# Optimization experiments

Hardware: AMD Instinct MI355X
Metric: run time of the kernel (lower is better)

Reference implementation:

```python
import jax, jax.numpy as jnp
import numpy as np

N = 50000
E = 625000
D = 128
L = 3
BN_EPS = 1e-5


def setup_inputs() -> dict:
    key = jax.random.key(0)
    ks = jax.random.split(key, 12)
    x = jax.random.normal(ks[0], (N, D), dtype=jnp.float32)
    edge_index = jax.random.randint(ks[1], (2, E), 0, N, dtype=jnp.int64)
    s = 1.0 / np.sqrt(D)
    W1 = jax.random.uniform(ks[2], (L, D, D), jnp.float32, -s, s)
    b1 = jax.random.uniform(ks[3], (L, D), jnp.float32, -s, s)
    W2 = jax.random.uniform(ks[4], (L, D, D), jnp.float32, -s, s)
    b2 = jax.random.uniform(ks[5], (L, D), jnp.float32, -s, s)
    eps = jnp.zeros((L,), jnp.float32)  # GINConv train_eps init 0
    gamma = jnp.ones((L, D), jnp.float32)
    beta = jnp.zeros((L, D), jnp.float32)
    Wl = jax.random.uniform(ks[6], (L, D, D), jnp.float32, -s, s)
    bl = jax.random.uniform(ks[7], (L, D), jnp.float32, -s, s)
    return {"x": x, "edge_index": edge_index, "W1": W1, "b1": b1, "W2": W2,
            "b2": b2, "eps": eps, "gamma": gamma, "beta": beta, "Wl": Wl, "bl": bl}


def reference(x, edge_index, W1, b1, W2, b2, eps, gamma, beta, Wl, bl):
    src, dst = edge_index[0], edge_index[1]
    xs = [x]
    h = x
    for i in range(L):
        # GIN aggregation: sum of neighbor (source) features at target nodes
        agg = jax.ops.segment_sum(h[src], dst, num_segments=N)  # [N, D]
        z = (1.0 + eps[i]) * h + agg
        # MLP: Linear -> ReLU -> Linear
        z = jax.nn.relu(z @ W1[i] + b1[i]) @ W2[i] + b2[i]
        # BatchNorm1d (training mode: batch stats, biased variance)
        mu = jnp.mean(z, axis=0)
        var = jnp.mean((z - mu) ** 2, axis=0)
        z = gamma[i] * (z - mu) * jax.lax.rsqrt(var + BN_EPS) + beta[i]
        if i != 0:
            z = z + xs[-1]
        h = jax.nn.relu(z)
        xs.append(h)
    outs = [xs[i + 1] @ Wl[i] + bl[i] for i in range(L)]
    return jnp.concatenate(outs, axis=-1)  # [N, L*D]
```

## Files before the change

kernel.cpp:

```cpp
#include <hip/hip_runtime.h>
#include <hip/hip_bf16.h>
#include <stdint.h>

#define NN 50000
#define NE 625000
#define DD 128
#define NL 3
#define GB 391

typedef __bf16 bf16x8 __attribute__((ext_vector_type(8)));
typedef float f32x4 __attribute__((ext_vector_type(4)));

__device__ __forceinline__ float bflo(uint32_t u) { return __uint_as_float(u << 16); }
__device__ __forceinline__ float bfhi(uint32_t u) { return __uint_as_float(u & 0xffff0000u); }
__device__ __forceinline__ uint16_t f2bf(float f) {
    __hip_bfloat16 h = __float2bfloat16(f);
    return __builtin_bit_cast(uint16_t, h);
}
__device__ __forceinline__ uint32_t pack2(float lo, float hi) {
    return (uint32_t)f2bf(lo) | ((uint32_t)f2bf(hi) << 16);
}

__global__ void k_hist(const int* __restrict__ dstv, int* __restrict__ deg) {
    int e = blockIdx.x * 256 + threadIdx.x;
    if (e < NE) atomicAdd(&deg[dstv[e]], 1);
}

__global__ __launch_bounds__(512) void k_bsum(const int* __restrict__ deg, int* __restrict__ bsum) {
    __shared__ int s[512];
    int i = blockIdx.x * 512 + threadIdx.x;
    int v = (i < NN) ? deg[i] : 0;
    s[threadIdx.x] = v;
    __syncthreads();
    for (int st = 256; st > 0; st >>= 1) {
        if (threadIdx.x < st) s[threadIdx.x] += s[threadIdx.x + st];
        __syncthreads();
    }
    if (threadIdx.x == 0) bsum[blockIdx.x] = s[0];
}

__global__ __launch_bounds__(128) void k_scanbs(const int* __restrict__ bsum, int* __restrict__ bsoff) {
    __shared__ int s[128];
    int t = threadIdx.x;
    int v = (t < 98) ? bsum[t] : 0;
    s[t] = v;
    __syncthreads();
    for (int st = 1; st < 128; st <<= 1) {
        int a = (t >= st) ? s[t - st] : 0;
        __syncthreads();
        s[t] += a;
        __syncthreads();
    }
    if (t < 98) bsoff[t] = s[t] - v;
}

__global__ __launch_bounds__(512) void k_scan2(int* __restrict__ deg_cursor,
                                               const int* __restrict__ bsoff,
                                               int* __restrict__ rowptr) {
    __shared__ int s[512];
    int t = threadIdx.x;
    int i = blockIdx.x * 512 + t;
    int v = (i < NN) ? deg_cursor[i] : 0;
    s[t] = v;
    __syncthreads();
    for (int st = 1; st < 512; st <<= 1) {
        int a = (t >= st) ? s[t - st] : 0;
        __syncthreads();
        s[t] += a;
        __syncthreads();
    }
    if (i < NN) {
        int excl = bsoff[blockIdx.x] + s[t] - v;
        rowptr[i] = excl;
        deg_cursor[i] = excl;
        if (i == NN - 1) rowptr[NN] = excl + v;
    }
}

__global__ void k_fill(const int* __restrict__ srcv, const int* __restrict__ dstv,
                       int* __restrict__ cursor, int* __restrict__ colv) {
    int e = blockIdx.x * 256 + threadIdx.x;
    if (e < NE) {
        int d = dstv[e];
        int p = atomicAdd(&cursor[d], 1);
        colv[p] = srcv[e];
    }
}

__global__ void k_convert_w(const float* __restrict__ W1, const float* __restrict__ W2,
                            const float* __restrict__ Wl, uint16_t* __restrict__ Wb) {
    int id = blockIdx.x * 256 + threadIdx.x;
    if (id >= 9 * 16384) return;
    int m = id >> 14;
    int r = id & 16383;
    int k = r >> 7;
    int col = r & 127;
    const float* src;
    if (m < 3) src = W1 + m * 16384;
    else if (m < 6) src = W2 + (m - 3) * 16384;
    else src = Wl + (m - 6) * 16384;
    float v = src[k * 128 + col];
    Wb[m * 16384 + col * 128 + (k ^ ((col & 7) << 3))] = f2bf(v);
}

__global__ void k_x2bf(const float* __restrict__ x, uint16_t* __restrict__ hb,
                       int* __restrict__ cursor) {
    int id = blockIdx.x * 256 + threadIdx.x;
    if (id < NN) cursor[id] = 0;
    int base = id * 4;
    if (base >= NN * DD) return;
    float4 v = *(const float4*)(x + base);
    uint2 st;
    st.x = pack2(v.x, v.y);
    st.y = pack2(v.z, v.w);
    *(uint2*)(hb + base) = st;
}

__global__ __launch_bounds__(256) void k_agg(const uint16_t* __restrict__ hb,
                                             const int* __restrict__ rowptr,
                                             const int* __restrict__ colv,
                                             const float* __restrict__ epsp, int layer,
                                             uint16_t* __restrict__ zb,
                                             float* __restrict__ bnsum) {
    if (blockIdx.x == 0) bnsum[threadIdx.x] = 0.f;
    int g = (blockIdx.x * 256 + threadIdx.x) >> 4;
    int l16 = threadIdx.x & 15;
    if (g >= NN) return;
    float onepe = 1.0f + epsp[layer];
    int beg = rowptr[g], end = rowptr[g + 1];
    const uint4* hp = (const uint4*)hb;
    float a0 = 0.f, a1 = 0.f, a2 = 0.f, a3 = 0.f, a4 = 0.f, a5 = 0.f, a6 = 0.f, a7 = 0.f;
    int j = beg;
    for (; j + 3 < end; j += 4) {
        int s0 = colv[j];
        int s1 = colv[j + 1];
        int s2 = colv[j + 2];
        int s3 = colv[j + 3];
        uint4 u0 = hp[(size_t)s0 * 16 + l16];
        uint4 u1 = hp[(size_t)s1 * 16 + l16];
        uint4 u2 = hp[(size_t)s2 * 16 + l16];
        uint4 u3 = hp[(size_t)s3 * 16 + l16];
        a0 += bflo(u0.x); a1 += bfhi(u0.x); a2 += bflo(u0.y); a3 += bfhi(u0.y);
        a4 += bflo(u0.z); a5 += bfhi(u0.z); a6 += bflo(u0.w); a7 += bfhi(u0.w);
        a0 += bflo(u1.x); a1 += bfhi(u1.x); a2 += bflo(u1.y); a3 += bfhi(u1.y);
        a4 += bflo(u1.z); a5 += bfhi(u1.z); a6 += bflo(u1.w); a7 += bfhi(u1.w);
        a0 += bflo(u2.x); a1 += bfhi(u2.x); a2 += bflo(u2.y); a3 += bfhi(u2.y);
        a4 += bflo(u2.z); a5 += bfhi(u2.z); a6 += bflo(u2.w); a7 += bfhi(u2.w);
        a0 += bflo(u3.x); a1 += bfhi(u3.x); a2 += bflo(u3.y); a3 += bfhi(u3.y);
        a4 += bflo(u3.z); a5 += bfhi(u3.z); a6 += bflo(u3.w); a7 += bfhi(u3.w);
    }
    for (; j < end; ++j) {
        int s0 = colv[j];
        uint4 u = hp[(size_t)s0 * 16 + l16];
        a0 += bflo(u.x); a1 += bfhi(u.x); a2 += bflo(u.y); a3 += bfhi(u.y);
        a4 += bflo(u.z); a5 += bfhi(u.z); a6 += bflo(u.w); a7 += bfhi(u.w);
    }
    uint4 hu = hp[(size_t)g * 16 + l16];
    a0 = fmaf(onepe, bflo(hu.x), a0); a1 = fmaf(onepe, bfhi(hu.x), a1);
    a2 = fmaf(onepe, bflo(hu.y), a2); a3 = fmaf(onepe, bfhi(hu.y), a3);
    a4 = fmaf(onepe, bflo(hu.z), a4); a5 = fmaf(onepe, bfhi(hu.z), a5);
    a6 = fmaf(onepe, bflo(hu.w), a6); a7 = fmaf(onepe, bfhi(hu.w), a7);
    uint4 st;
    st.x = pack2(a0, a1); st.y = pack2(a2, a3);
    st.z = pack2(a4, a5); st.w = pack2(a6, a7);
    ((uint4*)zb)[(size_t)g * 16 + l16] = st;
}

template <int MODE>
__global__ __launch_bounds__(256) void k_gemm(const uint16_t* __restrict__ A,
                                              const uint16_t* __restrict__ Wimg,
                                              const float* __restrict__ bias,
                                              float* __restrict__ bnsum,
                                              void* __restrict__ outp) {
    __shared__ uint16_t lds[16384];
    int tid = threadIdx.x;
    int wid = tid >> 6, lane = tid & 63;

#pragma unroll
    for (int it = 0; it < 8; ++it) {
        int idx = (it * 256 + tid) * 8;
        bf16x8 v = *(const bf16x8*)(Wimg + idx);
        *(bf16x8*)(&lds[idx]) = v;
    }
    __syncthreads();

    const int brow = blockIdx.x * 128;
    const int m0 = wid * 32;
    const int l15 = lane & 15;
    const int lhi = lane >> 4;

    f32x4 acc[2][8];
    f32x4 zero = {0.f, 0.f, 0.f, 0.f};
#pragma unroll
    for (int m = 0; m < 2; ++m)
#pragma unroll
        for (int n = 0; n < 8; ++n) acc[m][n] = zero;

    const char* Ab = (const char*)A;
#pragma unroll
    for (int kk = 0; kk < 4; ++kk) {
        int kbyte = kk * 64 + (lhi << 4);
        bf16x8 afrag[2];
#pragma unroll
        for (int m = 0; m < 2; ++m) {
            int row = brow + m0 + m * 16 + l15;
            if (row >= NN) row = NN - 1;
            afrag[m] = *(const bf16x8*)(Ab + (size_t)row * 256 + kbyte);
        }
#pragma unroll
        for (int n = 0; n < 8; ++n) {
            int col = n * 16 + l15;
            int addr = col * 256 + (kbyte ^ ((col & 7) << 4));
            bf16x8 bfrag = *(const bf16x8*)((const char*)lds + addr);
            acc[0][n] = __builtin_amdgcn_mfma_f32_16x16x32_bf16(afrag[0], bfrag, acc[0][n], 0, 0, 0);
            acc[1][n] = __builtin_amdgcn_mfma_f32_16x16x32_bf16(afrag[1], bfrag, acc[1][n], 0, 0, 0);
        }
    }

    float bcol[8];
#pragma unroll
    for (int n = 0; n < 8; ++n) bcol[n] = bias[n * 16 + l15];

    float s1[8], s2[8];
#pragma unroll
    for (int n = 0; n < 8; ++n) { s1[n] = 0.f; s2[n] = 0.f; }

#pragma unroll
    for (int m = 0; m < 2; ++m) {
        int rbase = brow + m0 + m * 16 + (lhi << 2);
#pragma unroll
        for (int r = 0; r < 4; ++r) {
            int row = rbase + r;
            bool ok = row < NN;
#pragma unroll
            for (int n = 0; n < 8; ++n) {
                float v = acc[m][n][r] + bcol[n];
                int col = n * 16 + l15;
                if (MODE == 0) {
                    v = fmaxf(v, 0.f);
                    if (ok) ((uint16_t*)outp)[(size_t)row * 128 + col] = f2bf(v);
                } else {
                    if (ok) {
                        ((float*)outp)[(size_t)row * 128 + col] = v;
                        s1[n] += v;
                        s2[n] += v * v;
                    }
                }
            }
        }
    }

    if (MODE == 1) {
        __syncthreads();
        float* ls = (float*)lds;
        ls[tid] = 0.f;
        __syncthreads();
#pragma unroll
        for (int n = 0; n < 8; ++n) {
            float a1 = s1[n] + __shfl_xor(s1[n], 16);
            a1 += __shfl_xor(a1, 32);
            float a2 = s2[n] + __shfl_xor(s2[n], 16);
            a2 += __shfl_xor(a2, 32);
            if (lane < 16) {
                atomicAdd(&ls[n * 16 + lane], a1);
                atomicAdd(&ls[128 + n * 16 + lane], a2);
            }
        }
        __syncthreads();
        atomicAdd(&bnsum[tid], ls[tid]);
    }
}

__global__ __launch_bounds__(256) void k_apply(const float* __restrict__ z2,
                                               const uint16_t* __restrict__ hin,
                                               const float* __restrict__ bnsum,
                                               const float* __restrict__ gamma,
                                               const float* __restrict__ beta, int layer,
                                               uint16_t* __restrict__ hout) {
    __shared__ float sA[128], sB[128];
    int tid = threadIdx.x;
    if (tid < 128) {
        float mu = bnsum[tid] * (1.0f / NN);
        float var = bnsum[128 + tid] * (1.0f / NN) - mu * mu;
        float a = gamma[layer * 128 + tid] * rsqrtf(var + 1e-5f);
        sA[tid] = a;
        sB[tid] = beta[layer * 128 + tid] - mu * a;
    }
    __syncthreads();
    int id = blockIdx.x * 256 + tid;
    int base = id * 4;
    if (base >= NN * DD) return;
    int c = base & 127;
    float4 z = *(const float4*)(z2 + base);
    float4 av = *(const float4*)(sA + c);
    float4 bv = *(const float4*)(sB + c);
    float v0 = fmaf(av.x, z.x, bv.x);
    float v1 = fmaf(av.y, z.y, bv.y);
    float v2 = fmaf(av.z, z.z, bv.z);
    float v3 = fmaf(av.w, z.w, bv.w);
    if (layer > 0) {
        uint2 h = *(const uint2*)(hin + base);
        v0 += bflo(h.x);
        v1 += bfhi(h.x);
        v2 += bflo(h.y);
        v3 += bfhi(h.y);
    }
    v0 = fmaxf(v0, 0.f);
    v1 = fmaxf(v1, 0.f);
    v2 = fmaxf(v2, 0.f);
    v3 = fmaxf(v3, 0.f);
    uint2 st;
    st.x = pack2(v0, v1);
    st.y = pack2(v2, v3);
    *(uint2*)(hout + base) = st;
}

__global__ __launch_bounds__(256) void k_outgemm(const uint16_t* __restrict__ h1,
                                                 const uint16_t* __restrict__ h2,
                                                 const uint16_t* __restrict__ h3,
                                                 const uint16_t* __restrict__ Wb6,
                                                 const float* __restrict__ bl,
                                                 float* __restrict__ out) {
    __shared__ uint16_t lds[16384];
    int layer = blockIdx.x / GB;
    int blk = blockIdx.x - layer * GB;
    const uint16_t* A = (layer == 0) ? h1 : ((layer == 1) ? h2 : h3);
    const uint16_t* Wimg = Wb6 + layer * 16384;
    const float* bias = bl + layer * 128;

    int tid = threadIdx.x;
    int wid = tid >> 6, lane = tid & 63;
#pragma unroll
    for (int it = 0; it < 8; ++it) {
        int idx = (it * 256 + tid) * 8;
        bf16x8 v = *(const bf16x8*)(Wimg + idx);
        *(bf16x8*)(&lds[idx]) = v;
    }
    __syncthreads();

    const int brow = blk * 128;
    const int m0 = wid * 32;
    const int l15 = lane & 15;
    const int lhi = lane >> 4;

    f32x4 acc[2][8];
    f32x4 zero = {0.f, 0.f, 0.f, 0.f};
#pragma unroll
    for (int m = 0; m < 2; ++m)
#pragma unroll
        for (int n = 0; n < 8; ++n) acc[m][n] = zero;

    const char* Ab = (const char*)A;
#pragma unroll
    for (int kk = 0; kk < 4; ++kk) {
        int kbyte = kk * 64 + (lhi << 4);
        bf16x8 afrag[2];
#pragma unroll
        for (int m = 0; m < 2; ++m) {
            int row = brow + m0 + m * 16 + l15;
            if (row >= NN) row = NN - 1;
            afrag[m] = *(const bf16x8*)(Ab + (size_t)row * 256 + kbyte);
        }
#pragma unroll
        for (int n = 0; n < 8; ++n) {
            int col = n * 16 + l15;
            int addr = col * 256 + (kbyte ^ ((col & 7) << 4));
            bf16x8 bfrag = *(const bf16x8*)((const char*)lds + addr);
            acc[0][n] = __builtin_amdgcn_mfma_f32_16x16x32_bf16(afrag[0], bfrag, acc[0][n], 0, 0, 0);
            acc[1][n] = __builtin_amdgcn_mfma_f32_16x16x32_bf16(afrag[1], bfrag, acc[1][n], 0, 0, 0);
        }
    }

    float bcol[8];
#pragma unroll
    for (int n = 0; n < 8; ++n) bcol[n] = bias[n * 16 + l15];

#pragma unroll
    for (int m = 0; m < 2; ++m) {
        int rbase = brow + m0 + m * 16 + (lhi << 2);
#pragma unroll
        for (int r = 0; r < 4; ++r) {
            int row = rbase + r;
            if (row < NN) {
#pragma unroll
                for (int n = 0; n < 8; ++n) {
                    float v = acc[m][n][r] + bcol[n];
                    out[(size_t)row * (NL * DD) + layer * 128 + n * 16 + l15] = v;
                }
            }
        }
    }
}

extern "C" void kernel_launch(void* const* d_in, const int* in_sizes, int n_in,
                              void* d_out, int out_size, void* d_ws, size_t ws_size,
                              hipStream_t stream) {
    const float* x = (const float*)d_in[0];
    const int* ei = (const int*)d_in[1];
    const float* W1 = (const float*)d_in[2];
    const float* b1 = (const float*)d_in[3];
    const float* W2 = (const float*)d_in[4];
    const float* b2 = (const float*)d_in[5];
    const float* epsp = (const float*)d_in[6];
    const float* gamma = (const float*)d_in[7];
    const float* beta = (const float*)d_in[8];
    const float* Wl = (const float*)d_in[9];
    const float* bl = (const float*)d_in[10];
    float* out = (float*)d_out;

    char* w = (char*)d_ws;
    size_t off = 0;
    auto take = [&](size_t b) -> char* {
        char* p = w + off;
        off += (b + 255) & ~(size_t)255;
        return p;
    };
    uint16_t* hb[4];
    for (int i = 0; i < 4; ++i) hb[i] = (uint16_t*)take((size_t)NN * DD * 2);
    uint16_t* zb = (uint16_t*)take((size_t)NN * DD * 2);
    uint16_t* t1b = (uint16_t*)take((size_t)NN * DD * 2);
    float* z2 = (float*)take((size_t)NN * DD * 4);
    int* rowptr = (int*)take((size_t)(NN + 1) * 4);
    int* cursor = (int*)take((size_t)NN * 4);
    int* colv = (int*)take((size_t)NE * 4);
    int* bsum = (int*)take(128 * 4);
    int* bsoff = (int*)take(128 * 4);
    uint16_t* Wb = (uint16_t*)take(9 * 16384 * 2);
    float* bnsum = (float*)take(256 * 4);

    const int* srcv = ei;
    const int* dstv = ei + NE;

    k_convert_w<<<(9 * 16384 + 255) / 256, 256, 0, stream>>>(W1, W2, Wl, Wb);
    k_x2bf<<<(NN * DD / 4 + 255) / 256, 256, 0, stream>>>(x, hb[0], cursor);

    k_hist<<<(NE + 255) / 256, 256, 0, stream>>>(dstv, cursor);
    k_bsum<<<98, 512, 0, stream>>>(cursor, bsum);
    k_scanbs<<<1, 128, 0, stream>>>(bsum, bsoff);
    k_scan2<<<98, 512, 0, stream>>>(cursor, bsoff, rowptr);
    k_fill<<<(NE + 255) / 256, 256, 0, stream>>>(srcv, dstv, cursor, colv);

    const int agg_blocks = (NN * 16 + 255) / 256;

    for (int l = 0; l < NL; ++l) {
        k_agg<<<agg_blocks, 256, 0, stream>>>(hb[l], rowptr, colv, epsp, l, zb, bnsum);
        k_gemm<0><<<GB, 256, 0, stream>>>(zb, Wb + l * 16384, b1 + l * 128, nullptr, t1b);
        k_gemm<1><<<GB, 256, 0, stream>>>(t1b, Wb + (3 + l) * 16384, b2 + l * 128, bnsum, z2);
        k_apply<<<(NN * DD / 4 + 255) / 256, 256, 0, stream>>>(z2, hb[l], bnsum, gamma, beta,
                                                               l, hb[l + 1]);
    }
    k_outgemm<<<NL * GB, 256, 0, stream>>>(hb[1], hb[2], hb[3], Wb + 6 * 16384, bl, out);
}
```

Measured before the change: 290.9 us.

## Fuse the two MLP GEMMs into one kernel with the intermediate kept in LDS

The two per-layer GEMM kernels (Linear+ReLU into a bf16 buffer, then Linear+bias+BN stats) become a single kernel. The ReLU output tile is written to a swizzled LDS buffer and read back as the A operand of the second GEMM. W2 is prefetched into registers and copied over the W1 LDS region once the first GEMM finishes. This removes the global write and read of the N×128 bf16 intermediate and one launch per layer, at the cost of doubling LDS per block (64KB) and adding register pressure, which may lower occupancy.

```diff
diff --git a/kernel.cpp b/kernel.cpp
--- a/kernel.cpp
+++ b/kernel.cpp
@@ -166,21 +166,26 @@
     ((uint4*)zb)[(size_t)g * 16 + l16] = st;
 }
 
-template <int MODE>
-__global__ __launch_bounds__(256) void k_gemm(const uint16_t* __restrict__ A,
-                                              const uint16_t* __restrict__ Wimg,
-                                              const float* __restrict__ bias,
-                                              float* __restrict__ bnsum,
-                                              void* __restrict__ outp) {
-    __shared__ uint16_t lds[16384];
+__global__ __launch_bounds__(256) void k_mlp(const uint16_t* __restrict__ A,
+                                             const uint16_t* __restrict__ W1img,
+                                             const uint16_t* __restrict__ W2img,
+                                             const float* __restrict__ b1,
+                                             const float* __restrict__ b2,
+                                             float* __restrict__ bnsum,
+                                             float* __restrict__ z2) {
+    __shared__ uint16_t ldsW[16384];
+    __shared__ uint16_t ldsT[16384];
     int tid = threadIdx.x;
     int wid = tid >> 6, lane = tid & 63;
 
+    bf16x8 w2r[8];
+#pragma unroll
+    for (int it = 0; it < 8; ++it) w2r[it] = *(const bf16x8*)(W2img + (it * 256 + tid) * 8);
+
 #pragma unroll
     for (int it = 0; it < 8; ++it) {
         int idx = (it * 256 + tid) * 8;
-        bf16x8 v = *(const bf16x8*)(Wimg + idx);
-        *(bf16x8*)(&lds[idx]) = v;
+        *(bf16x8*)(&ldsW[idx]) = *(const bf16x8*)(W1img + idx);
     }
     __syncthreads();
 
@@ -211,15 +216,65 @@
         for (int n = 0; n < 8; ++n) {
             int col = n * 16 + l15;
             int addr = col * 256 + (kbyte ^ ((col & 7) << 4));
-            bf16x8 bfrag = *(const bf16x8*)((const char*)lds + addr);
+            bf16x8 bfrag = *(const bf16x8*)((const char*)ldsW + addr);
             acc[0][n] = __builtin_amdgcn_mfma_f32_16x16x32_bf16(afrag[0], bfrag, acc[0][n], 0, 0, 0);
             acc[1][n] = __builtin_amdgcn_mfma_f32_16x16x32_bf16(afrag[1], bfrag, acc[1][n], 0, 0, 0);
         }
     }
 
-    float bcol[8];
-#pragma unroll
-    for (int n = 0; n < 8; ++n) bcol[n] = bias[n * 16 + l15];
+    {
+        float bc[8];
+#pragma unroll
+        for (int n = 0; n < 8; ++n) bc[n] = b1[n * 16 + l15];
+#pragma unroll
+        for (int m = 0; m < 2; ++m) {
+            int rbase = m0 + m * 16 + (lhi << 2);
+#pragma unroll
+            for (int r = 0; r < 4; ++r) {
+                int row = rbase + r;
+#pragma unroll
+                for (int n = 0; n < 8; ++n) {
+                    float v = fmaxf(acc[m][n][r] + bc[n], 0.f);
+                    int col = n * 16 + l15;
+                    int byteoff = row * 256 + ((col * 2) ^ ((row & 7) << 4));
+                    *(uint16_t*)((char*)ldsT + byteoff) = f2bf(v);
+                }
+            }
+        }
+    }
+    __syncthreads();
+
+#pragma unroll
+    for (int it = 0; it < 8; ++it) *(bf16x8*)(&ldsW[(it * 256 + tid) * 8]) = w2r[it];
+    __syncthreads();
+
+#pragma unroll
+    for (int m = 0; m < 2; ++m)
+#pragma unroll
+        for (int n = 0; n < 8; ++n) acc[m][n] = zero;
+
+#pragma unroll
+    for (int kk = 0; kk < 4; ++kk) {
+        int kbyte = kk * 64 + (lhi << 4);
+        bf16x8 afrag[2];
+#pragma unroll
+        for (int m = 0; m < 2; ++m) {
+            int rowl = m0 + m * 16 + l15;
+            afrag[m] = *(const bf16x8*)((const char*)ldsT + rowl * 256 + (kbyte ^ ((rowl & 7) << 4)));
+        }
+#pragma unroll
+        for (int n = 0; n < 8; ++n) {
+            int col = n * 16 + l15;
+            int addr = col * 256 + (kbyte ^ ((col & 7) << 4));
+            bf16x8 bfrag = *(const bf16x8*)((const char*)ldsW + addr);
+            acc[0][n] = __builtin_amdgcn_mfma_f32_16x16x32_bf16(afrag[0], bfrag, acc[0][n], 0, 0, 0);
+            acc[1][n] = __builtin_amdgcn_mfma_f32_16x16x32_bf16(afrag[1], bfrag, acc[1][n], 0, 0, 0);
+        }
+    }
+
+    float bc2[8];
+#pragma unroll
+    for (int n = 0; n < 8; ++n) bc2[n] = b2[n * 16 + l15];
 
     float s1[8], s2[8];
 #pragma unroll
@@ -234,41 +289,33 @@
             bool ok = row < NN;
 #pragma unroll
             for (int n = 0; n < 8; ++n) {
-                float v = acc[m][n][r] + bcol[n];
-                int col = n * 16 + l15;
-                if (MODE == 0) {
-                    v = fmaxf(v, 0.f);
-                    if (ok) ((uint16_t*)outp)[(size_t)row * 128 + col] = f2bf(v);
-                } else {
-                    if (ok) {
-                        ((float*)outp)[(size_t)row * 128 + col] = v;
-                        s1[n] += v;
-                        s2[n] += v * v;
-                    }
+                float v = acc[m][n][r] + bc2[n];
+                if (ok) {
+                    z2[(size_t)row * 128 + n * 16 + l15] = v;
+                    s1[n] += v;
+                    s2[n] += v * v;
                 }
             }
         }
     }
 
-    if (MODE == 1) {
-        __syncthreads();
-        float* ls = (float*)lds;
-        ls[tid] = 0.f;
-        __syncthreads();
-#pragma unroll
-        for (int n = 0; n < 8; ++n) {
-            float a1 = s1[n] + __shfl_xor(s1[n], 16);
-            a1 += __shfl_xor(a1, 32);
-            float a2 = s2[n] + __shfl_xor(s2[n], 16);
-            a2 += __shfl_xor(a2, 32);
-            if (lane < 16) {
-                atomicAdd(&ls[n * 16 + lane], a1);
-                atomicAdd(&ls[128 + n * 16 + lane], a2);
-            }
-        }
-        __syncthreads();
-        atomicAdd(&bnsum[tid], ls[tid]);
-    }
+    __syncthreads();
+    float* ls = (float*)ldsT;
+    ls[tid] = 0.f;
+    __syncthreads();
+#pragma unroll
+    for (int n = 0; n < 8; ++n) {
+        float a1 = s1[n] + __shfl_xor(s1[n], 16);
+        a1 += __shfl_xor(a1, 32);
+        float a2 = s2[n] + __shfl_xor(s2[n], 16);
+        a2 += __shfl_xor(a2, 32);
+        if (lane < 16) {
+            atomicAdd(&ls[n * 16 + lane], a1);
+            atomicAdd(&ls[128 + n * 16 + lane], a2);
+        }
+    }
+    __syncthreads();
+    atomicAdd(&bnsum[tid], ls[tid]);
 }
 
 __global__ __launch_bounds__(256) void k_apply(const float* __restrict__ z2,
@@ -418,7 +465,6 @@
     uint16_t* hb[4];
     for (int i = 0; i < 4; ++i) hb[i] = (uint16_t*)take((size_t)NN * DD * 2);
     uint16_t* zb = (uint16_t*)take((size_t)NN * DD * 2);
-    uint16_t* t1b = (uint16_t*)take((size_t)NN * DD * 2);
     float* z2 = (float*)take((size_t)NN * DD * 4);
     int* rowptr = (int*)take((size_t)(NN + 1) * 4);
     int* cursor = (int*)take((size_t)NN * 4);
@@ -444,8 +490,8 @@
 
     for (int l = 0; l < NL; ++l) {
         k_agg<<<agg_blocks, 256, 0, stream>>>(hb[l], rowptr, colv, epsp, l, zb, bnsum);
-        k_gemm<0><<<GB, 256, 0, stream>>>(zb, Wb + l * 16384, b1 + l * 128, nullptr, t1b);
-        k_gemm<1><<<GB, 256, 0, stream>>>(t1b, Wb + (3 + l) * 16384, b2 + l * 128, bnsum, z2);
+        k_mlp<<<GB, 256, 0, stream>>>(zb, Wb + l * 16384, Wb + (3 + l) * 16384,
+                                      b1 + l * 128, b2 + l * 128, bnsum, z2);
         k_apply<<<(NN * DD / 4 + 255) / 256, 256, 0, stream>>>(z2, hb[l], bnsum, gamma, beta,
                                                                l, hb[l + 1]);
     }
```

New measurement: 272.6 us. 6.3% less time.
